# Optimization experiments

Hardware: AMD Instinct MI355X
Metric: run time of the kernel (lower is better)

Reference implementation:

```python
import jax, jax.numpy as jnp
import numpy as np
from jax import lax


def _conv(x, w, b, padding):
    # x: NCHW, w: OIHW
    out = lax.conv_general_dilated(x, w, (1, 1), padding,
                                   dimension_numbers=('NCHW', 'OIHW', 'NCHW'))
    return out + b[None, :, None, None]


def _bilinear_sample(img, ys, xs):
    # img: [B,C,H,W]; ys, xs: [B,N] absolute pixel coords; zero padding outside.
    B, C, H, W = img.shape
    y0 = jnp.floor(ys); x0 = jnp.floor(xs)
    wy1 = ys - y0; wy0 = 1.0 - wy1
    wx1 = xs - x0; wx0 = 1.0 - wx1
    img_flat = img.reshape(B, C, H * W)

    def corner(yc, xc, w):
        valid = (yc >= 0) & (yc <= H - 1) & (xc >= 0) & (xc <= W - 1)
        yi = jnp.clip(yc, 0, H - 1).astype(jnp.int32)
        xi = jnp.clip(xc, 0, W - 1).astype(jnp.int32)
        idx = yi * W + xi  # [B,N]
        g = jax.vmap(lambda im, i: im[:, i])(img_flat, idx)  # [B,C,N]
        return g * (w * valid.astype(img.dtype))[:, None, :]

    return (corner(y0, x0, wy0 * wx0) + corner(y0, x0 + 1, wy0 * wx1)
            + corner(y0 + 1, x0, wy1 * wx0) + corner(y0 + 1, x0 + 1, wy1 * wx1))


def setup_inputs() -> dict:
    key = jax.random.key(0)
    ks = jax.random.split(key, 20)
    B, C, Co, H, W = 8, 64, 64, 128, 128
    f = jnp.float32

    def w_init(k, shape):
        fan_in = int(np.prod(shape[1:]))
        return jax.random.normal(k, shape, dtype=f) * (1.0 / np.sqrt(fan_in))

    inp = {
        'x': jax.random.normal(ks[0], (B, C, H, W), dtype=f),
        'offset': jax.random.normal(ks[1], (B, 18, H, W), dtype=f),
        # STN localization
        'stn_w1': w_init(ks[2], (32, C, 7, 7)), 'stn_b1': jnp.zeros((32,), f),
        'stn_w2': w_init(ks[3], (64, 32, 5, 5)), 'stn_b2': jnp.zeros((64,), f),
        'fc_w': jax.random.normal(ks[4], (6, 64), dtype=f) * 0.01,
        'fc_b': jnp.array([1, 0, 0, 0, 1, 0], f) + jax.random.normal(ks[5], (6,), dtype=f) * 0.02,
        # DeformConv2d
        'dcn_w': w_init(ks[6], (C, C, 3, 3)), 'dcn_b': jnp.zeros((C,), f),
        # weight_gen 1x1
        'wg_w': w_init(ks[7], (2, 2 * C, 1, 1)), 'wg_b': jnp.zeros((2,), f),
        # ELK block
        'w3': w_init(ks[8], (Co, C, 3, 3)), 'b3': jnp.zeros((Co,), f),
        'w15': w_init(ks[9], (Co, C, 1, 5)), 'b15': jnp.zeros((Co,), f),
        'w51': w_init(ks[10], (Co, C, 5, 1)), 'b51': jnp.zeros((Co,), f),
        'w1': w_init(ks[11], (Co, 3 * Co, 1, 1)), 'b1': jnp.zeros((Co,), f),
    }
    return inp


def _forward(x, offset, stn_w1, stn_b1, stn_w2, stn_b2, fc_w, fc_b,
             dcn_w, dcn_b, wg_w, wg_b, w3, b3, w15, b15, w51, b51, w1, b1):
    B, C, H, W = x.shape

    # ---- STN ----
    h = jax.nn.relu(_conv(x, stn_w1, stn_b1, [(3, 3), (3, 3)]))
    h = lax.reduce_window(h, -jnp.inf, lax.max, (1, 1, 2, 2), (1, 1, 2, 2), 'VALID')
    h = jax.nn.relu(_conv(h, stn_w2, stn_b2, [(2, 2), (2, 2)]))
    feat = h.mean(axis=(2, 3))  # AdaptiveAvgPool2d(1) -> [B,64]
    theta = (feat @ fc_w.T + fc_b).reshape(B, 2, 3)

    # affine_grid, align_corners=False
    xs_n = (2.0 * jnp.arange(W, dtype=x.dtype) + 1.0) / W - 1.0
    ys_n = (2.0 * jnp.arange(H, dtype=x.dtype) + 1.0) / H - 1.0
    Xn, Yn = jnp.meshgrid(xs_n, ys_n, indexing='xy')  # [H,W]
    gx = theta[:, 0, 0, None, None] * Xn + theta[:, 0, 1, None, None] * Yn + theta[:, 0, 2, None, None]
    gy = theta[:, 1, 0, None, None] * Xn + theta[:, 1, 1, None, None] * Yn + theta[:, 1, 2, None, None]
    # grid_sample unnormalize, align_corners=False
    ix = ((gx + 1.0) * W - 1.0) * 0.5
    iy = ((gy + 1.0) * H - 1.0) * 0.5
    Fs = _bilinear_sample(x, iy.reshape(B, -1), ix.reshape(B, -1)).reshape(B, C, H, W)

    # ---- DeformConv2d(k=3, pad=1): offset layout [.., 2k]=dy, [.., 2k+1]=dx ----
    off = offset.reshape(B, 9, 2, H, W)
    ki = (jnp.arange(9, dtype=x.dtype) // 3) - 1.0  # kernel dy
    kj = (jnp.arange(9, dtype=x.dtype) % 3) - 1.0   # kernel dx
    Yb = jnp.arange(H, dtype=x.dtype)[:, None]
    Xb = jnp.arange(W, dtype=x.dtype)[None, :]
    sy = Yb[None, None] + ki[None, :, None, None] + off[:, :, 0]  # [B,9,H,W]
    sx = Xb[None, None] + kj[None, :, None, None] + off[:, :, 1]
    samp = _bilinear_sample(x, sy.reshape(B, -1), sx.reshape(B, -1)).reshape(B, C, 9, H, W)
    Fd = jnp.einsum('bckhw,ock->bohw', samp, dcn_w.reshape(C, C, 9)) + dcn_b[None, :, None, None]

    # ---- weighted fusion ----
    weights = jax.nn.softmax(_conv(jnp.concatenate([Fs, Fd], 1), wg_w, wg_b, [(0, 0), (0, 0)]), axis=1)
    fused = Fs * weights[:, 0:1] + Fd * weights[:, 1:2]

    # ---- ELK block ----
    o1 = _conv(fused, w3, b3, [(1, 1), (1, 1)])
    o2 = _conv(fused, w15, b15, [(0, 0), (2, 2)])
    o3 = _conv(fused, w51, b51, [(2, 2), (0, 0)])
    return _conv(jnp.concatenate([o1, o2, o3], 1), w1, b1, [(0, 0), (0, 0)])


def reference(x, offset, stn_w1, stn_b1, stn_w2, stn_b2, fc_w, fc_b,
              dcn_w, dcn_b, wg_w, wg_b, w3, b3, w15, b15, w51, b51, w1, b1):
    return _forward(x, offset, stn_w1, stn_b1, stn_w2, stn_b2, fc_w, fc_b,
                    dcn_w, dcn_b, wg_w, wg_b, w3, b3, w15, b15, w51, b51, w1, b1)
```

## Files before the change

### kernel.cpp

```cpp
#include <hip/hip_runtime.h>
#include <math.h>

#define Bn 8
#define Cn 64
#define Hn 128
#define Wn 128
#define HWn 16384

typedef __attribute__((ext_vector_type(8))) __bf16 bf16x8;
typedef __attribute__((ext_vector_type(4))) __bf16 bf16x4;
typedef __attribute__((ext_vector_type(4))) float f32x4;

__device__ __forceinline__ int xcd_swz(int bid, int chunk) {
  return (bid & 7) * chunk + (bid >> 3);
}

__global__ __launch_bounds__(256) void k_wprep(
    const float* __restrict__ stn_w1, const float* __restrict__ dcn_w,
    const float* __restrict__ w1, const float* __restrict__ w3,
    const float* __restrict__ w15, const float* __restrict__ w51,
    const float* __restrict__ stn_w2,
    const float* __restrict__ b3, const float* __restrict__ b15,
    const float* __restrict__ b51, const float* __restrict__ b1,
    __bf16* __restrict__ wfrag, __bf16* __restrict__ dcnD,
    __bf16* __restrict__ weffD, __bf16* __restrict__ w2frag,
    float* __restrict__ beff, __bf16* __restrict__ p1T)
{
  int t = blockIdx.x * 256 + threadIdx.x;
  if (t < 100352) {
    int e = t & 7, l = (t >> 3) & 63, o16 = (t >> 9) & 1, ck = (t >> 10) & 1;
    int tap = t >> 11;
    int o = o16 * 16 + (l & 15), c = ck * 32 + (l >> 4) * 8 + e;
    wfrag[t] = (__bf16)stn_w1[(o * 64 + c) * 49 + tap];
    return;
  }
  t -= 100352;
  if (t < 36864) {
    int e = t & 7, l = (t >> 3) & 63, mf = (t >> 9) & 3, s = (t >> 11) & 1;
    int tap = t >> 12;
    int o = mf * 16 + (l & 15), c = s * 32 + (l >> 4) * 8 + e;
    dcnD[t] = (__bf16)dcn_w[(o * 64 + c) * 9 + tap];
    return;
  }
  t -= 36864;
  if (t < 53248) {
    const int DY[13] = {-2,-1,-1,-1, 0, 0, 0, 0, 0, 1, 1, 1, 2};
    const int DX[13] = { 0,-1, 0, 1,-2,-1, 0, 1, 2,-1, 0, 1, 0};
    int e = t & 7, l = (t >> 3) & 63, mf = (t >> 9) & 3, s = (t >> 11) & 1;
    int tap = t >> 12;
    int o = mf * 16 + (l & 15), c = s * 32 + (l >> 4) * 8 + e;
    int dy = DY[tap], dx = DX[tap];
    float v = 0.f;
    if (dy >= -1 && dy <= 1 && dx >= -1 && dx <= 1) {
      int k3 = (dy + 1) * 3 + (dx + 1);
      for (int m = 0; m < 64; m++) v = fmaf(w1[o * 192 + m], w3[(m * 64 + c) * 9 + k3], v);
    }
    if (dy == 0) {
      int k15 = dx + 2;
      for (int m = 0; m < 64; m++) v = fmaf(w1[o * 192 + 64 + m], w15[(m * 64 + c) * 5 + k15], v);
    }
    if (dx == 0) {
      int k51 = dy + 2;
      for (int m = 0; m < 64; m++) v = fmaf(w1[o * 192 + 128 + m], w51[(m * 64 + c) * 5 + k51], v);
    }
    weffD[t] = (__bf16)v;
    return;
  }
  t -= 53248;
  if (t < 51200) {
    int e = t & 7, l = (t >> 3) & 63, mf = (t >> 9) & 3;
    int tap = t >> 11;
    int o = mf * 16 + (l & 15), c = (l >> 4) * 8 + e;
    w2frag[t] = (__bf16)stn_w2[(o * 32 + c) * 25 + tap];
    return;
  }
  t -= 51200;
  if (t < 64) {
    float s = b1[t];
    for (int m = 0; m < 64; m++) {
      s = fmaf(w1[t * 192 + m],       b3[m],  s);
      s = fmaf(w1[t * 192 + 64 + m],  b15[m], s);
      s = fmaf(w1[t * 192 + 128 + m], b51[m], s);
    }
    beff[t] = s;
    return;
  }
  t -= 64;
  if (t < 73984) {
    bf16x8 z = {};
    *(bf16x8*)(p1T + (size_t)t * 16) = z;
    *(bf16x8*)(p1T + (size_t)t * 16 + 8) = z;
  }
}

__global__ __launch_bounds__(256) void k_xt(const float* __restrict__ x,
                                            __bf16* __restrict__ xT,
                                            __bf16* __restrict__ xC)
{
  int t = blockIdx.x * 256 + threadIdx.x;
  if (t >= 8 * 134 * 134 * 2) return;
  int half = t & 1;
  int p  = t >> 1;
  int wp = p % 134;
  int hp = (p / 134) % 134;
  int b  = p / (134 * 134);
  int h = hp - 3, w = wp - 3;
  bool inb = ((unsigned)h < 128u) && ((unsigned)w < 128u);
  const float* xb = x + (size_t)b * Cn * HWn + (size_t)(half * 32) * HWn + h * 128 + w;

  float v[32];
#pragma unroll
  for (int j = 0; j < 32; j++) v[j] = inb ? xb[(size_t)j * HWn] : 0.f;

  __bf16* dstT = xT + (size_t)p * 64 + half * 32;
#pragma unroll
  for (int g = 0; g < 4; g++) {
    bf16x8 r;
#pragma unroll
    for (int j = 0; j < 8; j++) r[j] = (__bf16)v[g * 8 + j];
    *(bf16x8*)(dstT + g * 8) = r;
    int oct = half * 4 + g;
    *(bf16x8*)(xC + ((((size_t)b * 8 + oct) * 134 + hp) * 144 + wp) * 8) = r;
  }
}

__global__ __launch_bounds__(256) void k_conv1m(
    const __bf16* __restrict__ xC, const __bf16* __restrict__ wfrag,
    const float* __restrict__ b1s, __bf16* __restrict__ p1T)
{
  __shared__ alignas(16) char tile[73728];
  const int lane = threadIdx.x & 63;
  const int wv   = threadIdx.x >> 6;
  const int swz  = xcd_swz(blockIdx.x, 64);
  const int b    = swz >> 6;
  const int h0   = (swz & 63) * 2;
  const int r    = wv >> 1;
  const int hf   = wv & 1;
  const int l15  = lane & 15;

  f32x4 acc[2][4];
#pragma unroll
  for (int o16 = 0; o16 < 2; o16++)
#pragma unroll
    for (int nf = 0; nf < 4; nf++) acc[o16][nf] = (f32x4){0.f, 0.f, 0.f, 0.f};

  const bf16x8* wf = (const bf16x8*)wfrag;
  const char* tb = (const char*)tile;
  const char* xCb = (const char*)xC;

  for (int ck = 0; ck < 2; ck++) {
    for (int i = wv; i < 72; i += 4) {
      int q = i / 18;
      int t = i - q * 18;
      const char* src = xCb
          + (((size_t)(b * 8 + ck * 4 + q) * 134 + h0) * 2304) + t * 1024 + lane * 16;
      char* dst = (char*)tile + i * 1024;
      __builtin_amdgcn_global_load_lds(
          (const __attribute__((address_space(1))) void*)src,
          (__attribute__((address_space(3))) void*)dst, 16, 0, 0);
    }
    __syncthreads();

    for (int tap = 0; tap < 49; tap++) {
      int dy7 = tap / 7;
      int dx7 = tap - dy7 * 7;
      bf16x8 a0 = wf[((tap * 2 + ck) * 2 + 0) * 64 + lane];
      bf16x8 a1 = wf[((tap * 2 + ck) * 2 + 1) * 64 + lane];
      const char* bp = tb + (lane >> 4) * 18432 + (r + dy7) * 2304
                          + (dx7 + hf * 64 + l15) * 16;
#pragma unroll
      for (int nf = 0; nf < 4; nf++) {
        bf16x8 bv = *(const bf16x8*)(bp + nf * 256);
        acc[0][nf] = __builtin_amdgcn_mfma_f32_16x16x32_bf16(a0, bv, acc[0][nf], 0, 0, 0);
        acc[1][nf] = __builtin_amdgcn_mfma_f32_16x16x32_bf16(a1, bv, acc[1][nf], 0, 0, 0);
      }
    }
    __syncthreads();
  }

#pragma unroll
  for (int o16 = 0; o16 < 2; o16++) {
    int ob = o16 * 16 + ((lane >> 4) << 2);
    float bb0 = b1s[ob], bb1 = b1s[ob + 1], bb2 = b1s[ob + 2], bb3 = b1s[ob + 3];
#pragma unroll
    for (int nf = 0; nf < 4; nf++) {
      int px = hf * 64 + nf * 16 + l15;
      bf16x4 rr;
      rr[0] = (__bf16)fmaxf(acc[o16][nf][0] + bb0, 0.f);
      rr[1] = (__bf16)fmaxf(acc[o16][nf][1] + bb1, 0.f);
      rr[2] = (__bf16)fmaxf(acc[o16][nf][2] + bb2, 0.f);
      rr[3] = (__bf16)fmaxf(acc[o16][nf][3] + bb3, 0.f);
      *(bf16x4*)((char*)tile + (size_t)(r * 128 + px) * 64 + ob * 2) = rr;
    }
  }
  __syncthreads();

  {
    int tid = threadIdx.x;
    int wp = tid >> 2, cg = tid & 3;
    const char* base = (const char*)tile;
    bf16x8 v00 = *(const bf16x8*)(base + (size_t)(0 * 128 + 2 * wp) * 64 + cg * 16);
    bf16x8 v01 = *(const bf16x8*)(base + (size_t)(0 * 128 + 2 * wp + 1) * 64 + cg * 16);
    bf16x8 v10 = *(const bf16x8*)(base + (size_t)(1 * 128 + 2 * wp) * 64 + cg * 16);
    bf16x8 v11 = *(const bf16x8*)(base + (size_t)(1 * 128 + 2 * wp + 1) * 64 + cg * 16);
    bf16x8 rr;
#pragma unroll
    for (int j = 0; j < 8; j++) {
      float m = fmaxf(fmaxf((float)v00[j], (float)v01[j]),
                      fmaxf((float)v10[j], (float)v11[j]));
      rr[j] = (__bf16)m;
    }
    int hp = (swz & 63) + 2;
    *(bf16x8*)(p1T + (((size_t)b * 68 + hp) * 68 + wp + 2) * 32 + cg * 8) = rr;
  }
}

__global__ __launch_bounds__(256) void k_conv2m(
    const __bf16* __restrict__ p1T, const __bf16* __restrict__ w2frag,
    const float* __restrict__ b2s, float* __restrict__ partial)
{
  __shared__ alignas(16) char tile[34816];
  __shared__ float sm2[4][16][64];
  const int lane = threadIdx.x & 63;
  const int wv   = threadIdx.x >> 6;
  const int b    = blockIdx.x >> 4;
  const int tl   = blockIdx.x & 15;
  const int h0   = tl * 4;
  const int l15  = lane & 15;

  f32x4 acc[4][4];
#pragma unroll
  for (int mf = 0; mf < 4; mf++)
#pragma unroll
    for (int nf = 0; nf < 4; nf++) acc[mf][nf] = (f32x4){0.f, 0.f, 0.f, 0.f};

  const char* src0 = (const char*)p1T + (((size_t)b * 68 + h0) * 68) * 64;
  for (int i = wv; i < 34; i += 4) {
    __builtin_amdgcn_global_load_lds(
        (const __attribute__((address_space(1))) void*)(src0 + i * 1024 + lane * 16),
        (__attribute__((address_space(3))) void*)((char*)tile + i * 1024), 16, 0, 0);
  }
  __syncthreads();

  const bf16x8* wf = (const bf16x8*)w2frag;
  const char* tb = (const char*)tile;
  for (int tap = 0; tap < 25; tap++) {
    int ky = tap / 5, kx = tap - ky * 5;
    bf16x8 a0 = wf[(tap * 4 + 0) * 64 + lane];
    bf16x8 a1 = wf[(tap * 4 + 1) * 64 + lane];
    bf16x8 a2 = wf[(tap * 4 + 2) * 64 + lane];
    bf16x8 a3 = wf[(tap * 4 + 3) * 64 + lane];
    const char* bp = tb + (((wv + ky) * 68 + kx + l15) * 64) + (lane >> 4) * 16;
#pragma unroll
    for (int nf = 0; nf < 4; nf++) {
      bf16x8 bv = *(const bf16x8*)(bp + nf * 1024);
      acc[0][nf] = __builtin_amdgcn_mfma_f32_16x16x32_bf16(a0, bv, acc[0][nf], 0, 0, 0);
      acc[1][nf] = __builtin_amdgcn_mfma_f32_16x16x32_bf16(a1, bv, acc[1][nf], 0, 0, 0);
      acc[2][nf] = __builtin_amdgcn_mfma_f32_16x16x32_bf16(a2, bv, acc[2][nf], 0, 0, 0);
      acc[3][nf] = __builtin_amdgcn_mfma_f32_16x16x32_bf16(a3, bv, acc[3][nf], 0, 0, 0);
    }
  }

#pragma unroll
  for (int mf = 0; mf < 4; mf++) {
    int ob = mf * 16 + ((lane >> 4) << 2);
#pragma unroll
    for (int rr = 0; rr < 4; rr++) {
      float bb = b2s[ob + rr];
      float s = 0.f;
#pragma unroll
      for (int nf = 0; nf < 4; nf++)
        s += fmaxf(acc[mf][nf][rr] + bb, 0.f);
      sm2[wv][l15][ob + rr] = s;
    }
  }
  __syncthreads();
  if (threadIdx.x < 64) {
    float s = 0.f;
#pragma unroll
    for (int w2 = 0; w2 < 4; w2++)
      for (int l = 0; l < 16; l++) s += sm2[w2][l][threadIdx.x];
    partial[(size_t)(b * 16 + tl) * 64 + threadIdx.x] = s;
  }
}

__global__ __launch_bounds__(512) void k_theta(
    const float* __restrict__ partial, const float* __restrict__ fc_w,
    const float* __restrict__ fc_b, float* __restrict__ theta)
{
  __shared__ float featL[512];
  int tid = threadIdx.x;
  {
    int b = tid >> 6, co = tid & 63;
    float s = 0.f;
#pragma unroll
    for (int t = 0; t < 16; t++) s += partial[(size_t)(b * 16 + t) * 64 + co];
    featL[tid] = s;
  }
  __syncthreads();
  if (tid < 48) {
    int b = tid / 6, i = tid - b * 6;
    float s = 0.f;
    for (int k = 0; k < 64; k++) s = fmaf(featL[b * 64 + k], fc_w[i * 64 + k], s);
    theta[tid] = fmaf(s, 1.f / 4096.f, fc_b[i]);
  }
}

__device__ __forceinline__ void bilin_setup(
    const __bf16* __restrict__ xb, float sy, float sx,
    const __bf16*& c00, const __bf16*& c01,
    const __bf16*& c10, const __bf16*& c11,
    float& w00, float& w01, float& w10, float& w11)
{
  float y0f = floorf(sy), x0f = floorf(sx);
  float wy1 = sy - y0f, wy0 = 1.f - wy1;
  float wx1 = sx - x0f, wx0 = 1.f - wx1;
  bool vy0 = (y0f >= 0.f) && (y0f <= 127.f);
  bool vy1 = (y0f >= -1.f) && (y0f <= 126.f);
  bool vx0 = (x0f >= 0.f) && (x0f <= 127.f);
  bool vx1 = (x0f >= -1.f) && (x0f <= 126.f);
  int yi0 = (int)fminf(fmaxf(y0f, 0.f), 127.f);
  int yi1 = (int)fminf(fmaxf(y0f + 1.f, 0.f), 127.f);
  int xi0 = (int)fminf(fmaxf(x0f, 0.f), 127.f);
  int xi1 = (int)fminf(fmaxf(x0f + 1.f, 0.f), 127.f);
  w00 = wy0 * wx0 * ((vy0 && vx0) ? 1.f : 0.f);
  w01 = wy0 * wx1 * ((vy0 && vx1) ? 1.f : 0.f);
  w10 = wy1 * wx0 * ((vy1 && vx0) ? 1.f : 0.f);
  w11 = wy1 * wx1 * ((vy1 && vx1) ? 1.f : 0.f);
  c00 = xb + ((size_t)((yi0 + 3) * 134) + xi0 + 3) * 64;
  c01 = xb + ((size_t)((yi0 + 3) * 134) + xi1 + 3) * 64;
  c10 = xb + ((size_t)((yi1 + 3) * 134) + xi0 + 3) * 64;
  c11 = xb + ((size_t)((yi1 + 3) * 134) + xi1 + 3) * 64;
}

__global__ __launch_bounds__(64) void k_dcnm(
    const __bf16* __restrict__ xT, const float* __restrict__ off,
    const float* __restrict__ theta,
    const __bf16* __restrict__ dcnD, const float* __restrict__ dcn_b,
    __bf16* __restrict__ FdT, __bf16* __restrict__ FsT)
{
  __shared__ alignas(16) char smem[2][2048];
  const int lane = threadIdx.x;
  const int swz  = xcd_swz(blockIdx.x, 1024);
  const int b    = swz >> 10;
  const int rem  = swz & 1023;
  const int h    = rem >> 3;
  const int px0  = (rem & 7) * 16;
  const int l15  = lane & 15;
  const int g    = lane >> 4;
  const int pg   = lane >> 2;
  const int q    = lane & 3;
  const int wg   = px0 + pg;

  const __bf16* xb = xT + (size_t)b * 134 * 134 * 64;

  const float* ob = off + (size_t)b * 18 * HWn + h * 128 + wg;
  float offs[18];
#pragma unroll
  for (int i = 0; i < 18; i++) offs[i] = ob[(size_t)i * HWn];

  {
    const float* t = theta + b * 6;
    float xn = (float)(2 * wg + 1) * (1.f / 128.f) - 1.f;
    float yn = (float)(2 * h + 1) * (1.f / 128.f) - 1.f;
    float gxv = t[0] * xn + t[1] * yn + t[2];
    float gyv = t[3] * xn + t[4] * yn + t[5];
    float ix = fmaf(gxv, 64.f, 63.5f);
    float iy = fmaf(gyv, 64.f, 63.5f);
    const __bf16 *c00, *c01, *c10, *c11;
    float w00, w01, w10, w11;
    bilin_setup(xb, iy, ix, c00, c01, c10, c11, w00, w01, w10, w11);
    __bf16* dst = FsT + ((size_t)b * HWn + h * 128 + wg) * 64;
#pragma unroll
    for (int s = 0; s < 2; s++) {
      int eo = q * 8 + s * 32;
      bf16x8 v00 = *(const bf16x8*)(c00 + eo);
      bf16x8 v01 = *(const bf16x8*)(c01 + eo);
      bf16x8 v10 = *(const bf16x8*)(c10 + eo);
      bf16x8 v11 = *(const bf16x8*)(c11 + eo);
      bf16x8 r;
#pragma unroll
      for (int j = 0; j < 8; j++) {
        float f = w00 * (float)v00[j] + w01 * (float)v01[j]
                + w10 * (float)v10[j] + w11 * (float)v11[j];
        r[j] = (__bf16)f;
      }
      *(bf16x8*)(dst + eo) = r;
    }
  }

  f32x4 acc[4];
#pragma unroll
  for (int mf = 0; mf < 4; mf++) acc[mf] = (f32x4){0.f, 0.f, 0.f, 0.f};
  const bf16x8* aD = (const bf16x8*)dcnD;

#pragma unroll
  for (int k = 0; k < 9; k++) {
    char* sm = smem[k & 1];
    float sy = (float)(h + k / 3 - 1) + offs[2 * k];
    float sx = (float)(wg + k % 3 - 1) + offs[2 * k + 1];
    const __bf16 *c00, *c01, *c10, *c11;
    float w00, w01, w10, w11;
    bilin_setup(xb, sy, sx, c00, c01, c10, c11, w00, w01, w10, w11);

#pragma unroll
    for (int s = 0; s < 2; s++) {
      int eo = q * 8 + s * 32;
      bf16x8 v00 = *(const bf16x8*)(c00 + eo);
      bf16x8 v01 = *(const bf16x8*)(c01 + eo);
      bf16x8 v10 = *(const bf16x8*)(c10 + eo);
      bf16x8 v11 = *(const bf16x8*)(c11 + eo);
      bf16x8 r;
#pragma unroll
      for (int j = 0; j < 8; j++) {
        float f = w00 * (float)v00[j] + w01 * (float)v01[j]
                + w10 * (float)v10[j] + w11 * (float)v11[j];
        r[j] = (__bf16)f;
      }
      int c = s * 4 + q;
      *(bf16x8*)(sm + pg * 128 + ((c ^ (pg & 7)) * 16)) = r;
    }

#pragma unroll
    for (int s = 0; s < 2; s++) {
      int c = s * 4 + g;
      bf16x8 a = *(const bf16x8*)(sm + l15 * 128 + ((c ^ (l15 & 7)) * 16));
      acc[0] = __builtin_amdgcn_mfma_f32_16x16x32_bf16(
          a, aD[((k * 2 + s) * 4 + 0) * 64 + lane], acc[0], 0, 0, 0);
      acc[1] = __builtin_amdgcn_mfma_f32_16x16x32_bf16(
          a, aD[((k * 2 + s) * 4 + 1) * 64 + lane], acc[1], 0, 0, 0);
      acc[2] = __builtin_amdgcn_mfma_f32_16x16x32_bf16(
          a, aD[((k * 2 + s) * 4 + 2) * 64 + lane], acc[2], 0, 0, 0);
      acc[3] = __builtin_amdgcn_mfma_f32_16x16x32_bf16(
          a, aD[((k * 2 + s) * 4 + 3) * 64 + lane], acc[3], 0, 0, 0);
    }
  }

  __bf16* fb = FdT + ((size_t)b * HWn + h * 128 + px0) * 64;
#pragma unroll
  for (int mf = 0; mf < 4; mf++) {
    int o = mf * 16 + l15;
    float bias = dcn_b[o];
#pragma unroll
    for (int r = 0; r < 4; r++) {
      int pxl = g * 4 + r;
      fb[(size_t)pxl * 64 + o] = (__bf16)(acc[mf][r] + bias);
    }
  }
}

#define FPL ((size_t)132 * 132 * 8)
__global__ __launch_bounds__(256) void k_fuseT(
    const __bf16* __restrict__ FsT, const __bf16* __restrict__ FdT,
    const float* __restrict__ wg_w, const float* __restrict__ wg_b,
    __bf16* __restrict__ fusedT)
{
  int id = blockIdx.x * 256 + threadIdx.x;
  if (id >= 8 * 132 * 132) return;
  int wp = id % 132;
  int hp = (id / 132) % 132;
  int b  = id / (132 * 132);
  size_t ppix = (size_t)(hp * 132 + wp) * 8;
  int h = hp - 2, w = wp - 2;
  if (((unsigned)h >= 128u) || ((unsigned)w >= 128u)) {
    bf16x8 z = {};
#pragma unroll
    for (int oct = 0; oct < 8; oct++)
      *(bf16x8*)(fusedT + ((size_t)b * 8 + oct) * FPL + ppix) = z;
    return;
  }
  const bf16x8* fs = (const bf16x8*)(FsT + ((size_t)b * HWn + h * 128 + w) * 64);
  const bf16x8* fd = (const bf16x8*)(FdT + ((size_t)b * HWn + h * 128 + w) * 64);
  bf16x8 fsv[8], fdv[8];
  float s0 = wg_b[0], s1 = wg_b[1];
#pragma unroll
  for (int oct = 0; oct < 8; oct++) {
    fsv[oct] = fs[oct];
    fdv[oct] = fd[oct];
#pragma unroll
    for (int j = 0; j < 8; j++) {
      int c = oct * 8 + j;
      float a = (float)fsv[oct][j], d = (float)fdv[oct][j];
      s0 = fmaf(wg_w[c],       a, fmaf(wg_w[64 + c],  d, s0));
      s1 = fmaf(wg_w[128 + c], a, fmaf(wg_w[192 + c], d, s1));
    }
  }
  float p0 = 1.f / (1.f + __expf(s1 - s0));
  float p1 = 1.f - p0;
#pragma unroll
  for (int oct = 0; oct < 8; oct++) {
    bf16x8 r;
#pragma unroll
    for (int j = 0; j < 8; j++)
      r[j] = (__bf16)(p0 * (float)fsv[oct][j] + p1 * (float)fdv[oct][j]);
    *(bf16x8*)(fusedT + ((size_t)b * 8 + oct) * FPL + ppix) = r;
  }
}

__global__ __launch_bounds__(256) void k_elkm(
    const __bf16* __restrict__ fusedT, const __bf16* __restrict__ weffD,
    const float* __restrict__ beff, float* __restrict__ out)
{
  const int DY[13] = {-2,-1,-1,-1, 0, 0, 0, 0, 0, 1, 1, 1, 2};
  const int DX[13] = { 0,-1, 0, 1,-2,-1, 0, 1, 2,-1, 0, 1, 0};
  const int lane = threadIdx.x & 63;
  const int wv   = threadIdx.x >> 6;
  const int swz  = xcd_swz(blockIdx.x, 64);
  const int b    = swz >> 6;
  const int h    = (swz & 63) * 2 + (wv >> 1);
  const int half = wv & 1;
  const int l15  = lane & 15;
  const int g    = lane >> 4;

  f32x4 acc[4][4];
#pragma unroll
  for (int mf = 0; mf < 4; mf++)
#pragma unroll
    for (int nf = 0; nf < 4; nf++) acc[mf][nf] = (f32x4){0.f, 0.f, 0.f, 0.f};

  const bf16x8* aD = (const bf16x8*)weffD;
  const __bf16* pl0 = fusedT + ((size_t)b * 8 + g) * FPL;
  const __bf16* pl1 = pl0 + 4 * FPL;

  for (int t = 0; t < 13; t++) {
    int hp = h + 2 + DY[t];
    size_t rowb = (size_t)(hp * 132 + half * 64 + 2 + DX[t] + l15) * 8;
#pragma unroll
    for (int s = 0; s < 2; s++) {
      const __bf16* pl = s ? pl1 : pl0;
      bf16x8 a0 = aD[((t * 2 + s) * 4 + 0) * 64 + lane];
      bf16x8 a1 = aD[((t * 2 + s) * 4 + 1) * 64 + lane];
      bf16x8 a2 = aD[((t * 2 + s) * 4 + 2) * 64 + lane];
      bf16x8 a3 = aD[((t * 2 + s) * 4 + 3) * 64 + lane];
#pragma unroll
      for (int nf = 0; nf < 4; nf++) {
        bf16x8 bv = *(const bf16x8*)(pl + rowb + (size_t)nf * 128);
        acc[0][nf] = __builtin_amdgcn_mfma_f32_16x16x32_bf16(a0, bv, acc[0][nf], 0, 0, 0);
        acc[1][nf] = __builtin_amdgcn_mfma_f32_16x16x32_bf16(a1, bv, acc[1][nf], 0, 0, 0);
        acc[2][nf] = __builtin_amdgcn_mfma_f32_16x16x32_bf16(a2, bv, acc[2][nf], 0, 0, 0);
        acc[3][nf] = __builtin_amdgcn_mfma_f32_16x16x32_bf16(a3, bv, acc[3][nf], 0, 0, 0);
      }
    }
  }

#pragma unroll
  for (int mf = 0; mf < 4; mf++) {
    int ob = mf * 16 + (g << 2);
#pragma unroll
    for (int r = 0; r < 4; r++) {
      int o = ob + r;
      float bb = beff[o];
      float* orow = out + ((size_t)(b * 64 + o)) * HWn + h * 128 + half * 64 + l15;
#pragma unroll
      for (int nf = 0; nf < 4; nf++)
        orow[nf * 16] = acc[mf][nf][r] + bb;
    }
  }
}

extern "C" void kernel_launch(void* const* d_in, const int* in_sizes, int n_in,
                              void* d_out, int out_size, void* d_ws, size_t ws_size,
                              hipStream_t stream)
{
  (void)in_sizes; (void)n_in; (void)out_size; (void)ws_size;
  const float* x      = (const float*)d_in[0];
  const float* offset = (const float*)d_in[1];
  const float* stn_w1 = (const float*)d_in[2];
  const float* stn_b1 = (const float*)d_in[3];
  const float* stn_w2 = (const float*)d_in[4];
  const float* stn_b2 = (const float*)d_in[5];
  const float* fc_w   = (const float*)d_in[6];
  const float* fc_b   = (const float*)d_in[7];
  const float* dcn_w  = (const float*)d_in[8];
  const float* dcn_b  = (const float*)d_in[9];
  const float* wg_w   = (const float*)d_in[10];
  const float* wg_b   = (const float*)d_in[11];
  const float* w3     = (const float*)d_in[12];
  const float* b3     = (const float*)d_in[13];
  const float* w15    = (const float*)d_in[14];
  const float* b15    = (const float*)d_in[15];
  const float* w51    = (const float*)d_in[16];
  const float* b51    = (const float*)d_in[17];
  const float* w1     = (const float*)d_in[18];
  const float* b1     = (const float*)d_in[19];

  float* ws      = (float*)d_ws;
  __bf16* xT     = (__bf16*)ws;
  __bf16* fusedT = (__bf16*)ws;
  __bf16* xC     = (__bf16*)(ws + 4596736);
  __bf16* FsT    = (__bf16*)(ws + 4596736);
  __bf16* FdT    = (__bf16*)(ws + 9536512);
  __bf16* p1T    = (__bf16*)(ws + 11633664);
  float*  partial= ws + 12225536;
  float*  theta  = ws + 14323200;
  __bf16* wfrag  = (__bf16*)(ws + 14323264);
  __bf16* w2frag = (__bf16*)(ws + 14373440);
  float*  beff   = ws + 14399040;
  __bf16* dcnD   = (__bf16*)(ws + 14399104);
  __bf16* weffD  = (__bf16*)(ws + 14417536);
  float*  out    = (float*)d_out;

  k_wprep <<<1234, 256, 0, stream>>>(stn_w1, dcn_w, w1, w3, w15, w51, stn_w2,
                                     b3, b15, b51, b1,
                                     wfrag, dcnD, weffD, w2frag, beff, p1T);
  k_xt    <<<1123, 256, 0, stream>>>(x, xT, xC);
  k_conv1m<<<512,  256, 0, stream>>>(xC, wfrag, stn_b1, p1T);
  k_conv2m<<<128,  256, 0, stream>>>(p1T, w2frag, stn_b2, partial);
  k_theta <<<1,    512, 0, stream>>>(partial, fc_w, fc_b, theta);
  k_dcnm  <<<8192, 64,  0, stream>>>(xT, offset, theta, dcnD, dcn_b, FdT, FsT);
  k_fuseT <<<545,  256, 0, stream>>>(FsT, FdT, wg_w, wg_b, fusedT);
  k_elkm  <<<512,  256, 0, stream>>>(fusedT, weffD, beff, out);
}
```

Baseline: 179.0 us.

## Fuse softmax-weighted fusion into deformable conv kernel and zero only padding borders

Drops the separate fuse kernel. The deform-conv kernel now computes the 1x1 weight-gen logits for Fs and Fd with cross-lane shuffles, applies the two-way softmax, and writes the fused padded tensor directly. A small new kernel zeroes only the border of the padded buffer. This removes the global write and re-read of the FsT and FdT intermediates, at the cost of extra shuffles, shared-memory staging and more register pressure in the deform kernel.

```diff
diff --git a/kernel.cpp b/kernel.cpp
--- a/kernel.cpp
+++ b/kernel.cpp
@@ -91,6 +91,29 @@
     *(bf16x8*)(p1T + (size_t)t * 16) = z;
     *(bf16x8*)(p1T + (size_t)t * 16 + 8) = z;
   }
+}
+
+#define FPL ((size_t)132 * 132 * 8)
+__global__ __launch_bounds__(256) void k_zpad(__bf16* __restrict__ fusedT)
+{
+  int t = blockIdx.x * 256 + threadIdx.x;
+  if (t >= 66560) return;
+  int pp = t % 1040;
+  int po = (t / 1040) & 7;
+  int b  = t / 8320;
+  int row, col;
+  if (pp < 528) {
+    int rr = pp / 132;
+    row = (rr < 2) ? rr : 128 + rr;
+    col = pp % 132;
+  } else {
+    int q2 = pp - 528;
+    row = 2 + (q2 >> 2);
+    int cs = q2 & 3;
+    col = (cs < 2) ? cs : 128 + cs;
+  }
+  bf16x8 z = {};
+  *(bf16x8*)(fusedT + ((size_t)b * 8 + po) * FPL + ((size_t)(row * 132 + col)) * 8) = z;
 }
 
 __global__ __launch_bounds__(256) void k_xt(const float* __restrict__ x,
@@ -337,7 +360,8 @@
     const __bf16* __restrict__ xT, const float* __restrict__ off,
     const float* __restrict__ theta,
     const __bf16* __restrict__ dcnD, const float* __restrict__ dcn_b,
-    __bf16* __restrict__ FdT, __bf16* __restrict__ FsT)
+    const float* __restrict__ wg_w, const float* __restrict__ wg_b,
+    __bf16* __restrict__ fusedT)
 {
   __shared__ alignas(16) char smem[2][2048];
   const int lane = threadIdx.x;
@@ -359,6 +383,8 @@
 #pragma unroll
   for (int i = 0; i < 18; i++) offs[i] = ob[(size_t)i * HWn];
 
+  bf16x8 fs0c, fs1c;
+  float s0s = 0.f, s1s = 0.f;
   {
     const float* t = theta + b * 6;
     float xn = (float)(2 * wg + 1) * (1.f / 128.f) - 1.f;
@@ -370,23 +396,40 @@
     const __bf16 *c00, *c01, *c10, *c11;
     float w00, w01, w10, w11;
     bilin_setup(xb, iy, ix, c00, c01, c10, c11, w00, w01, w10, w11);
-    __bf16* dst = FsT + ((size_t)b * HWn + h * 128 + wg) * 64;
-#pragma unroll
-    for (int s = 0; s < 2; s++) {
-      int eo = q * 8 + s * 32;
+    {
+      int eo = q * 8;
       bf16x8 v00 = *(const bf16x8*)(c00 + eo);
       bf16x8 v01 = *(const bf16x8*)(c01 + eo);
       bf16x8 v10 = *(const bf16x8*)(c10 + eo);
       bf16x8 v11 = *(const bf16x8*)(c11 + eo);
-      bf16x8 r;
 #pragma unroll
       for (int j = 0; j < 8; j++) {
         float f = w00 * (float)v00[j] + w01 * (float)v01[j]
                 + w10 * (float)v10[j] + w11 * (float)v11[j];
-        r[j] = (__bf16)f;
+        fs0c[j] = (__bf16)f;
       }
-      *(bf16x8*)(dst + eo) = r;
-    }
+    }
+    {
+      int eo = q * 8 + 32;
+      bf16x8 v00 = *(const bf16x8*)(c00 + eo);
+      bf16x8 v01 = *(const bf16x8*)(c01 + eo);
+      bf16x8 v10 = *(const bf16x8*)(c10 + eo);
+      bf16x8 v11 = *(const bf16x8*)(c11 + eo);
+#pragma unroll
+      for (int j = 0; j < 8; j++) {
+        float f = w00 * (float)v00[j] + w01 * (float)v01[j]
+                + w10 * (float)v10[j] + w11 * (float)v11[j];
+        fs1c[j] = (__bf16)f;
+      }
+    }
+#pragma unroll
+    for (int j = 0; j < 8; j++) {
+      float f0 = (float)fs0c[j], f1 = (float)fs1c[j];
+      s0s = fmaf(wg_w[q * 8 + j],       f0, fmaf(wg_w[32 + q * 8 + j],  f1, s0s));
+      s1s = fmaf(wg_w[128 + q * 8 + j], f0, fmaf(wg_w[160 + q * 8 + j], f1, s1s));
+    }
+    s0s += __shfl_xor(s0s, 1); s0s += __shfl_xor(s0s, 2);
+    s1s += __shfl_xor(s1s, 1); s1s += __shfl_xor(s1s, 2);
   }
 
   f32x4 acc[4];
@@ -436,65 +479,77 @@
     }
   }
 
-  __bf16* fb = FdT + ((size_t)b * HWn + h * 128 + px0) * 64;
+  float fdb_f[4][4];
+  float s0d[4] = {0.f, 0.f, 0.f, 0.f};
+  float s1d[4] = {0.f, 0.f, 0.f, 0.f};
 #pragma unroll
   for (int mf = 0; mf < 4; mf++) {
     int o = mf * 16 + l15;
     float bias = dcn_b[o];
+    float w0 = wg_w[64 + o], w1 = wg_w[192 + o];
 #pragma unroll
     for (int r = 0; r < 4; r++) {
-      int pxl = g * 4 + r;
-      fb[(size_t)pxl * 64 + o] = (__bf16)(acc[mf][r] + bias);
-    }
-  }
-}
-
-#define FPL ((size_t)132 * 132 * 8)
-__global__ __launch_bounds__(256) void k_fuseT(
-    const __bf16* __restrict__ FsT, const __bf16* __restrict__ FdT,
-    const float* __restrict__ wg_w, const float* __restrict__ wg_b,
-    __bf16* __restrict__ fusedT)
-{
-  int id = blockIdx.x * 256 + threadIdx.x;
-  if (id >= 8 * 132 * 132) return;
-  int wp = id % 132;
-  int hp = (id / 132) % 132;
-  int b  = id / (132 * 132);
-  size_t ppix = (size_t)(hp * 132 + wp) * 8;
-  int h = hp - 2, w = wp - 2;
-  if (((unsigned)h >= 128u) || ((unsigned)w >= 128u)) {
-    bf16x8 z = {};
-#pragma unroll
-    for (int oct = 0; oct < 8; oct++)
-      *(bf16x8*)(fusedT + ((size_t)b * 8 + oct) * FPL + ppix) = z;
-    return;
-  }
-  const bf16x8* fs = (const bf16x8*)(FsT + ((size_t)b * HWn + h * 128 + w) * 64);
-  const bf16x8* fd = (const bf16x8*)(FdT + ((size_t)b * HWn + h * 128 + w) * 64);
-  bf16x8 fsv[8], fdv[8];
-  float s0 = wg_b[0], s1 = wg_b[1];
-#pragma unroll
-  for (int oct = 0; oct < 8; oct++) {
-    fsv[oct] = fs[oct];
-    fdv[oct] = fd[oct];
-#pragma unroll
-    for (int j = 0; j < 8; j++) {
-      int c = oct * 8 + j;
-      float a = (float)fsv[oct][j], d = (float)fdv[oct][j];
-      s0 = fmaf(wg_w[c],       a, fmaf(wg_w[64 + c],  d, s0));
-      s1 = fmaf(wg_w[128 + c], a, fmaf(wg_w[192 + c], d, s1));
-    }
-  }
-  float p0 = 1.f / (1.f + __expf(s1 - s0));
+      __bf16 fb = (__bf16)(acc[mf][r] + bias);
+      float fv = (float)fb;
+      fdb_f[mf][r] = fv;
+      s0d[r] = fmaf(w0, fv, s0d[r]);
+      s1d[r] = fmaf(w1, fv, s1d[r]);
+    }
+  }
+#pragma unroll
+  for (int m = 1; m < 16; m <<= 1) {
+#pragma unroll
+    for (int r = 0; r < 4; r++) {
+      s0d[r] += __shfl_xor(s0d[r], m);
+      s1d[r] += __shfl_xor(s1d[r], m);
+    }
+  }
+
+  float p0v0, p0v1, p0v2, p0v3;
+  {
+    float ss0, ss1, S0, S1;
+    ss0 = __shfl(s0s, (g * 4 + 0) * 4); ss1 = __shfl(s1s, (g * 4 + 0) * 4);
+    S0 = ss0 + s0d[0] + wg_b[0]; S1 = ss1 + s1d[0] + wg_b[1];
+    p0v0 = 1.f / (1.f + __expf(S1 - S0));
+    ss0 = __shfl(s0s, (g * 4 + 1) * 4); ss1 = __shfl(s1s, (g * 4 + 1) * 4);
+    S0 = ss0 + s0d[1] + wg_b[0]; S1 = ss1 + s1d[1] + wg_b[1];
+    p0v1 = 1.f / (1.f + __expf(S1 - S0));
+    ss0 = __shfl(s0s, (g * 4 + 2) * 4); ss1 = __shfl(s1s, (g * 4 + 2) * 4);
+    S0 = ss0 + s0d[2] + wg_b[0]; S1 = ss1 + s1d[2] + wg_b[1];
+    p0v2 = 1.f / (1.f + __expf(S1 - S0));
+    ss0 = __shfl(s0s, (g * 4 + 3) * 4); ss1 = __shfl(s1s, (g * 4 + 3) * 4);
+    S0 = ss0 + s0d[3] + wg_b[0]; S1 = ss1 + s1d[3] + wg_b[1];
+    p0v3 = 1.f / (1.f + __expf(S1 - S0));
+  }
+
+  __bf16* fdb16 = (__bf16*)smem[0];
+#pragma unroll
+  for (int mf = 0; mf < 4; mf++) {
+    bf16x4 v;
+#pragma unroll
+    for (int r = 0; r < 4; r++) v[r] = (__bf16)fdb_f[mf][r];
+    *(bf16x4*)(fdb16 + (mf * 16 + l15) * 16 + g * 4) = v;
+  }
+  float* p0b = (float*)smem[1];
+  if (l15 == 0) p0b[g * 4 + 0] = p0v0;
+  if (l15 == 1) p0b[g * 4 + 1] = p0v1;
+  if (l15 == 2) p0b[g * 4 + 2] = p0v2;
+  if (l15 == 3) p0b[g * 4 + 3] = p0v3;
+
+  float p0 = p0b[pg];
   float p1 = 1.f - p0;
-#pragma unroll
-  for (int oct = 0; oct < 8; oct++) {
-    bf16x8 r;
-#pragma unroll
-    for (int j = 0; j < 8; j++)
-      r[j] = (__bf16)(p0 * (float)fsv[oct][j] + p1 * (float)fdv[oct][j]);
-    *(bf16x8*)(fusedT + ((size_t)b * 8 + oct) * FPL + ppix) = r;
-  }
+
+  bf16x8 o0, o1;
+#pragma unroll
+  for (int j = 0; j < 8; j++) {
+    float fd0 = (float)fdb16[(q * 8 + j) * 16 + pg];
+    float fd1 = (float)fdb16[(32 + q * 8 + j) * 16 + pg];
+    o0[j] = (__bf16)(p0 * (float)fs0c[j] + p1 * fd0);
+    o1[j] = (__bf16)(p0 * (float)fs1c[j] + p1 * fd1);
+  }
+  size_t ppix = (size_t)((h + 2) * 132 + wg + 2) * 8;
+  *(bf16x8*)(fusedT + ((size_t)b * 8 + q) * FPL + ppix) = o0;
+  *(bf16x8*)(fusedT + ((size_t)b * 8 + 4 + q) * FPL + ppix) = o1;
 }
 
 __global__ __launch_bounds__(256) void k_elkm(
@@ -586,10 +641,8 @@
 
   float* ws      = (float*)d_ws;
   __bf16* xT     = (__bf16*)ws;
-  __bf16* fusedT = (__bf16*)ws;
   __bf16* xC     = (__bf16*)(ws + 4596736);
-  __bf16* FsT    = (__bf16*)(ws + 4596736);
-  __bf16* FdT    = (__bf16*)(ws + 9536512);
+  __bf16* fusedT = (__bf16*)(ws + 4596736);
   __bf16* p1T    = (__bf16*)(ws + 11633664);
   float*  partial= ws + 12225536;
   float*  theta  = ws + 14323200;
@@ -607,7 +660,8 @@
   k_conv1m<<<512,  256, 0, stream>>>(xC, wfrag, stn_b1, p1T);
   k_conv2m<<<128,  256, 0, stream>>>(p1T, w2frag, stn_b2, partial);
   k_theta <<<1,    512, 0, stream>>>(partial, fc_w, fc_b, theta);
-  k_dcnm  <<<8192, 64,  0, stream>>>(xT, offset, theta, dcnD, dcn_b, FdT, FsT);
-  k_fuseT <<<545,  256, 0, stream>>>(FsT, FdT, wg_w, wg_b, fusedT);
+  k_zpad  <<<260,  256, 0, stream>>>(fusedT);
+  k_dcnm  <<<8192, 64,  0, stream>>>(xT, offset, theta, dcnD, dcn_b,
+                                     wg_w, wg_b, fusedT);
   k_elkm  <<<512,  256, 0, stream>>>(fusedT, weffD, beff, out);
 }
```

Result: faster. 168.1 us (-6.1%).
